# Performance work log

Measured on AMD Instinct MI355X. Metric: run time of the kernel, lower is better.

## Reference

```python
import jax, jax.numpy as jnp
import numpy as np
import math

B, L, H, NH = 4, 2048, 256, 8
DH = H // NH

def setup_inputs() -> dict:
    key = jax.random.key(0)
    ks = jax.random.split(key, 10)
    q = jax.random.normal(ks[0], (B, L, H), dtype=jnp.float32)
    k = jax.random.normal(ks[1], (B, L, H), dtype=jnp.float32)
    v = jax.random.normal(ks[2], (B, L, H), dtype=jnp.float32)
    k_b = jax.random.normal(ks[3], (B, L, H), dtype=jnp.float32)
    mask = jnp.ones((B, L), dtype=jnp.int32)
    # learned params
    scale_w = jax.random.normal(ks[4], (NH, L), dtype=jnp.float32)
    Wb = jax.random.normal(ks[5], (H, H), dtype=jnp.float32) * (1.0 / math.sqrt(H))
    bb = jnp.zeros((H,), dtype=jnp.float32)
    Ww = jax.random.normal(ks[6], (H, H), dtype=jnp.float32) * (1.0 / math.sqrt(H))
    bw = jnp.zeros((H,), dtype=jnp.float32)
    return {"q": q, "k": k, "v": v, "k_b": k_b, "mask": mask,
            "scale_w": scale_w, "Wb": Wb, "bb": bb, "Ww": Ww, "bw": bw}

def _split_heads(x):
    b, l, _ = x.shape
    return x.reshape(b, l, NH, DH).transpose(0, 2, 1, 3)  # [B, NH, L, DH]

def reference(q, k, v, k_b, mask, scale_w, Wb, bb, Ww, bw):
    qh = _split_heads(q)
    kh = _split_heads(k)
    vh = _split_heads(v)
    kb = _split_heads(k_b @ Wb.T + bb)
    # dual QK^T: [B, NH, L, L]
    corr = jnp.einsum('bhqd,bhkd->bhqk', qh, kh) + jnp.einsum('bhqd,bhkd->bhqk', qh, kb)
    corr = corr * (1.0 / math.sqrt(DH))
    # per-head, per-query-position learned scale
    corr = corr * scale_w[None, :, :, None]
    # mask over key positions: [B,1,1,L]
    corr = jnp.where(mask[:, None, None, :] == 0, jnp.float32(-1e9), corr)
    prob = jax.nn.softmax(corr, axis=-1)
    hidden = jnp.einsum('bhqk,bhkd->bhqd', prob, vh)  # [B, NH, L, DH]
    hidden = hidden.transpose(0, 2, 1, 3).reshape(hidden.shape[0], -1, NH * DH)
    return hidden @ Ww.T + bw
```

## Files before the change

kernel.cpp:

```cpp
#include <hip/hip_runtime.h>
#include <stdint.h>
#include <stddef.h>


#define B_ 4
#define L_ 2048
#define H_ 256
#define NH_ 8
#define DH_ 32

typedef float    f32x4  __attribute__((ext_vector_type(4)));
typedef float    f32x16 __attribute__((ext_vector_type(16)));
typedef __bf16   bf16x8 __attribute__((ext_vector_type(8)));
typedef uint16_t u16x4  __attribute__((ext_vector_type(4)));
typedef uint16_t u16x8  __attribute__((ext_vector_type(8)));

static __device__ __forceinline__ uint16_t f2bf(float f) {
  __bf16 h = (__bf16)f;
  return __builtin_bit_cast(uint16_t, h);
}

static __device__ __forceinline__ void gl16(const void* g, void* l) {
  __builtin_amdgcn_global_load_lds(
      (const __attribute__((address_space(1))) uint32_t*)g,
      (__attribute__((address_space(3))) uint32_t*)l, 16, 0, 0);
}

#define OFF_KSUM 0
#define OFF_VTP  (OFF_KSUM + (size_t)B_*NH_*L_*DH_*2)
#define OFF_HID  (OFF_VTP  + (size_t)B_*NH_*L_*DH_*2)


__global__ __launch_bounds__(256, 2) void wv_k(const float* __restrict__ v,
                                               uint16_t* __restrict__ vtp) {
  __shared__ uint16_t T[128][33];
  const int tid = threadIdx.x;
  const int bh = blockIdx.x >> 4, t = blockIdx.x & 15;
  const int b = bh >> 3, h = bh & 7;
  {
    int r = tid >> 1, half = tid & 1;
    const float* src = v + ((size_t)(b * 2048 + t * 128 + r)) * 256 + h * 32 + half * 16;
    f32x4 s0 = *(const f32x4*)(src);
    f32x4 s1 = *(const f32x4*)(src + 4);
    f32x4 s2 = *(const f32x4*)(src + 8);
    f32x4 s3 = *(const f32x4*)(src + 12);
#pragma unroll
    for (int i = 0; i < 4; i++) {
      T[r][half * 16 + i]      = f2bf(s0[i]);
      T[r][half * 16 + 4 + i]  = f2bf(s1[i]);
      T[r][half * 16 + 8 + i]  = f2bf(s2[i]);
      T[r][half * 16 + 12 + i] = f2bf(s3[i]);
    }
  }
  __syncthreads();
#pragma unroll
  for (int rep = 0; rep < 2; rep++) {
    int gid = rep * 256 + tid;
    int slot = gid >> 5, d = gid & 31;
    int kg = slot >> 2, s = (slot >> 1) & 1, hii = slot & 1;
    u16x8 val;
#pragma unroll
    for (int e = 0; e < 8; e++) {
      int key = kg * 32 + s * 16 + 4 * hii + (e & 3) + 8 * (e >> 2);
      val[e] = T[key][d];
    }
    *(u16x8*)(vtp + (size_t)bh * 65536 + t * 4096 + slot * 256 + d * 8) = val;
  }
}

__global__ __launch_bounds__(512, 1) void ksum_k(const float* __restrict__ kb,
                                                 const float* __restrict__ wb,
                                                 const float* __restrict__ kin,
                                                 const float* __restrict__ bb,
                                                 uint16_t* __restrict__ ksum_out) {
  __shared__ uint16_t WB[65536];
  const int tid = threadIdx.x;
  const int mblk = blockIdx.x;
  const int wv = tid >> 6, lane = tid & 63;
  const int g = lane >> 4, qi = lane & 15;
  const int rt = wv & 1, ch = wv >> 1;
  const int m = mblk * 32 + rt * 16 + qi;
  const int n0 = ch * 64;

#pragma unroll
  for (int s = 0; s < 16; s++) {
    int gid = s * 512 + tid;
    int n = gid >> 5, gl = gid & 31;
    const float* src = wb + (size_t)n * 256 + gl * 8;
    f32x4 a0 = *(const f32x4*)src;
    f32x4 a1 = *(const f32x4*)(src + 4);
    u16x8 val;
#pragma unroll
    for (int i = 0; i < 4; i++) { val[i] = f2bf(a0[i]); val[4 + i] = f2bf(a1[i]); }
    *(u16x8*)&WB[n * 256 + (gl ^ (n & 7)) * 8] = val;
  }
  __syncthreads();

  f32x4 acc[4];
#pragma unroll
  for (int i = 0; i < 4; i++) acc[i] = (f32x4){0.f, 0.f, 0.f, 0.f};

#pragma unroll
  for (int ks = 0; ks < 8; ks++) {
    const float* ap = kb + (size_t)m * 256 + ks * 32 + g * 8;
    f32x4 a0 = *(const f32x4*)ap;
    f32x4 a1 = *(const f32x4*)(ap + 4);
    bf16x8 af;
#pragma unroll
    for (int i = 0; i < 4; i++) { af[i] = (__bf16)a0[i]; af[4 + i] = (__bf16)a1[i]; }
#pragma unroll
    for (int nt = 0; nt < 4; nt++) {
      int n = n0 + nt * 16 + qi;
      bf16x8 bf = *(const bf16x8*)&WB[n * 256 + ((ks * 4 + g) ^ (n & 7)) * 8];
      acc[nt] = __builtin_amdgcn_mfma_f32_16x16x32_bf16(af, bf, acc[nt], 0, 0, 0);
    }
  }
#pragma unroll
  for (int nt = 0; nt < 4; nt++) {
    int n = n0 + nt * 16 + qi;
    float bbv = bb[n];
    int h = n >> 5, d = n & 31;
#pragma unroll
    for (int j = 0; j < 4; j++) {
      int mr = mblk * 32 + rt * 16 + g * 4 + j;
      float val = acc[nt][j] + bbv + kin[(size_t)mr * 256 + n];
      int bq = mr >> 11, l = mr & 2047;
      size_t off = (size_t)(bq * 8 + h) * 65536 +
                   (l >> 5) * 1024 + (d >> 4) * 512 + (l & 31) * 16 + (d & 15);
      ksum_out[off] = f2bf(val);
    }
  }
}

__global__ __launch_bounds__(512, 2) void attn_k(const float* __restrict__ q,
                                                 const int* __restrict__ mask,
                                                 const float* __restrict__ scale_w,
                                                 const uint16_t* __restrict__ ksum,
                                                 const uint16_t* __restrict__ vtp,
                                                 uint16_t* __restrict__ hid) {
  __shared__ __align__(16) uint16_t KV[2][8192];
  __shared__ int anyz;

  const int bid = blockIdx.x;
  const int bh = bid & 31, qblk = bid >> 5;
  const int b = bh >> 3, h = bh & 7;
  const int tid = threadIdx.x, wv = tid >> 6, lane = tid & 63;
  const int qi = lane & 31, hi = lane >> 5;
  const int qrow = qblk * 256 + wv * 32 + qi;

  const float scale = scale_w[h * 2048 + qrow] * (0.17677669529663687f * 1.4426950408889634f);
  const float* qp = q + ((size_t)(b * 2048 + qrow)) * 256 + h * 32;
  bf16x8 qf0, qf1;
  {
    f32x4 a0 = *(const f32x4*)(qp + hi * 8);
    f32x4 a1 = *(const f32x4*)(qp + hi * 8 + 4);
    f32x4 c0 = *(const f32x4*)(qp + 16 + hi * 8);
    f32x4 c1 = *(const f32x4*)(qp + 16 + hi * 8 + 4);
#pragma unroll
    for (int i = 0; i < 4; i++) {
      qf0[i] = (__bf16)(a0[i] * scale); qf0[4 + i] = (__bf16)(a1[i] * scale);
      qf1[i] = (__bf16)(c0[i] * scale); qf1[4 + i] = (__bf16)(c1[i] * scale);
    }
  }

  const uint16_t* kbase = ksum + (size_t)bh * 65536;
  const uint16_t* vbase = vtp + (size_t)bh * 65536;

  if (tid == 0) anyz = 0;
  __syncthreads();
  {
    int bad = 0;
#pragma unroll
    for (int i = 0; i < 4; i++) bad |= (mask[b * 2048 + tid * 4 + i] == 0);
    if (bad) anyz = 1;
  }
  __syncthreads();
  const bool allmask = (anyz == 0);

#define STAGE(tt, bufp)                                                            \
  {                                                                                \
    gl16(kbase + (tt) * 4096 + wv * 512 + lane * 8, (bufp) + wv * 512);            \
    gl16(vbase + (tt) * 4096 + wv * 512 + lane * 8, (bufp) + 4096 + wv * 512);     \
  }
  STAGE(0, &KV[0][0]);
  STAGE(1, &KV[1][0]);

  float lsa[4] = {0.f, 0.f, 0.f, 0.f};
  f32x16 Oa, Ob, Z0;
#pragma unroll
  for (int i = 0; i < 16; i++) { Oa[i] = 0.f; Ob[i] = 0.f; Z0[i] = 0.f; }

  for (int t = 0; t < 16; t++) {
    uint16_t* bufp = &KV[t & 1][0];
    if (t < 15) { asm volatile("s_waitcnt vmcnt(2)" ::: "memory"); }
    else        { asm volatile("s_waitcnt vmcnt(0)" ::: "memory"); }
    __builtin_amdgcn_sched_barrier(0);
    __builtin_amdgcn_s_barrier();

    const uint16_t* Kl = bufp;
    const uint16_t* Vl = bufp + 4096;
#pragma unroll
    for (int kg = 0; kg < 4; kg++) {
      bf16x8 kf0 = *(const bf16x8*)&Kl[kg * 1024 + qi * 16 + hi * 8];
      bf16x8 kf1 = *(const bf16x8*)&Kl[kg * 1024 + 512 + qi * 16 + hi * 8];
      f32x16 S;
      __builtin_amdgcn_s_setprio(1);
      S = __builtin_amdgcn_mfma_f32_32x32x16_bf16(kf0, qf0, Z0, 0, 0, 0);
      S = __builtin_amdgcn_mfma_f32_32x32x16_bf16(kf1, qf1, S, 0, 0, 0);
      __builtin_amdgcn_s_setprio(0);

      if (!allmask) {
        const int* mrow = mask + b * 2048 + t * 128 + kg * 32 + 4 * hi;
#pragma unroll
        for (int r = 0; r < 16; r++)
          if (mrow[(r & 3) + 8 * (r >> 2)] == 0) S[r] = -1.0e9f;
      }

      bf16x8 pa0, pa1;
#pragma unroll
      for (int r = 0; r < 8; r++) {
        float p = __builtin_amdgcn_exp2f(S[r]);
        pa0[r] = (__bf16)p;
        lsa[r & 3] += p;
      }
#pragma unroll
      for (int r = 0; r < 8; r++) {
        float p = __builtin_amdgcn_exp2f(S[8 + r]);
        pa1[r] = (__bf16)p;
        lsa[r & 3] += p;
      }

      bf16x8 vf0 = *(const bf16x8*)&Vl[(kg * 4 + hi) * 256 + qi * 8];
      bf16x8 vf1 = *(const bf16x8*)&Vl[(kg * 4 + 2 + hi) * 256 + qi * 8];
      __builtin_amdgcn_s_setprio(1);
      Oa = __builtin_amdgcn_mfma_f32_32x32x16_bf16(vf0, pa0, Oa, 0, 0, 0);
      Ob = __builtin_amdgcn_mfma_f32_32x32x16_bf16(vf1, pa1, Ob, 0, 0, 0);
      __builtin_amdgcn_s_setprio(0);
    }

    __builtin_amdgcn_s_barrier();
    if (t < 14) STAGE(t + 2, bufp);
  }
#undef STAGE

  float l = (lsa[0] + lsa[1]) + (lsa[2] + lsa[3]);
  l += __shfl_xor(l, 32);
  const float inv = 1.0f / l;
  uint16_t* hp = hid + ((size_t)(b * 2048 + qrow)) * 256 + h * 32;
#pragma unroll
  for (int grp = 0; grp < 4; grp++) {
    u16x4 st;
#pragma unroll
    for (int j = 0; j < 4; j++) st[j] = f2bf((Oa[grp * 4 + j] + Ob[grp * 4 + j]) * inv);
    *(u16x4*)(hp + grp * 8 + hi * 4) = st;
  }
}

__global__ __launch_bounds__(512, 1) void oproj_k(const uint16_t* __restrict__ hid,
                                                  const float* __restrict__ ww,
                                                  const float* __restrict__ bw,
                                                  float* __restrict__ out) {
  __shared__ uint16_t WW[65536];
  const int tid = threadIdx.x;
  const int mblk = blockIdx.x;
  const int wv = tid >> 6, lane = tid & 63;
  const int g = lane >> 4, qi = lane & 15;
  const int rt = wv & 1, ch = wv >> 1;
  const int m = mblk * 32 + rt * 16 + qi;
  const int n0 = ch * 64;

#pragma unroll
  for (int s = 0; s < 16; s++) {
    int gid = s * 512 + tid;
    int n = gid >> 5, gl = gid & 31;
    const float* src = ww + (size_t)n * 256 + gl * 8;
    f32x4 a0 = *(const f32x4*)src;
    f32x4 a1 = *(const f32x4*)(src + 4);
    u16x8 val;
#pragma unroll
    for (int i = 0; i < 4; i++) { val[i] = f2bf(a0[i]); val[4 + i] = f2bf(a1[i]); }
    *(u16x8*)&WW[n * 256 + (gl ^ (n & 7)) * 8] = val;
  }
  __syncthreads();

  f32x4 acc[4];
#pragma unroll
  for (int i = 0; i < 4; i++) acc[i] = (f32x4){0.f, 0.f, 0.f, 0.f};

#pragma unroll
  for (int ks = 0; ks < 8; ks++) {
    bf16x8 af = *(const bf16x8*)(hid + (size_t)m * 256 + ks * 32 + g * 8);
#pragma unroll
    for (int nt = 0; nt < 4; nt++) {
      int n = n0 + nt * 16 + qi;
      bf16x8 bf = *(const bf16x8*)&WW[n * 256 + ((ks * 4 + g) ^ (n & 7)) * 8];
      acc[nt] = __builtin_amdgcn_mfma_f32_16x16x32_bf16(af, bf, acc[nt], 0, 0, 0);
    }
  }
#pragma unroll
  for (int nt = 0; nt < 4; nt++) {
    int n = n0 + nt * 16 + qi;
    float bwv = bw[n];
#pragma unroll
    for (int j = 0; j < 4; j++) {
      int mr = mblk * 32 + rt * 16 + g * 4 + j;
      out[(size_t)mr * 256 + n] = acc[nt][j] + bwv;
    }
  }
}

extern "C" void kernel_launch(void* const* d_in, const int* in_sizes, int n_in,
                              void* d_out, int out_size, void* d_ws, size_t ws_size,
                              hipStream_t stream) {
  const float* q       = (const float*)d_in[0];
  const float* k       = (const float*)d_in[1];
  const float* v       = (const float*)d_in[2];
  const float* kb      = (const float*)d_in[3];
  const int*   mask    = (const int*)d_in[4];
  const float* scale_w = (const float*)d_in[5];
  const float* Wb      = (const float*)d_in[6];
  const float* bb      = (const float*)d_in[7];
  const float* Ww      = (const float*)d_in[8];
  const float* bw      = (const float*)d_in[9];

  char* ws = (char*)d_ws;
  uint16_t* ksum  = (uint16_t*)(ws + OFF_KSUM);
  uint16_t* vtp   = (uint16_t*)(ws + OFF_VTP);
  uint16_t* hid   = (uint16_t*)(ws + OFF_HID);
  float* out = (float*)d_out;

  wv_k<<<dim3(512), dim3(256), 0, stream>>>(v, vtp);
  ksum_k<<<dim3(256), dim3(512), 0, stream>>>(kb, Wb, k, bb, ksum);
  attn_k<<<dim3(256), dim3(512), 0, stream>>>(q, mask, scale_w, ksum, vtp, hid);
  oproj_k<<<dim3(256), dim3(512), 0, stream>>>(hid, Ww, bw, out);
}
```

Measured before the change: 52.03 us.

## Merge V-transpose and K-sum prep kernels; halve attention block size

Folds the V transpose/convert kernel into the K-sum projection kernel as extra blocks of a single launch, removing one kernel launch and letting both workloads run concurrently. The attention kernel now uses 256-thread blocks covering 128 query rows each, doubling the grid to 512 blocks for better CU coverage, with each wave issuing twice as many async K/V stage loads and waiting on a larger vmcnt. The V blocks now carry the large 128KB LDS allocation sized for the GEMM path, which may limit their occupancy. Halving the block size also doubles total K/V tile traffic per head.

```diff
diff --git a/kernel.cpp b/kernel.cpp
--- a/kernel.cpp
+++ b/kernel.cpp
@@ -31,51 +31,48 @@
 #define OFF_HID  (OFF_VTP  + (size_t)B_*NH_*L_*DH_*2)
 
 
-__global__ __launch_bounds__(256, 2) void wv_k(const float* __restrict__ v,
-                                               uint16_t* __restrict__ vtp) {
-  __shared__ uint16_t T[128][33];
-  const int tid = threadIdx.x;
-  const int bh = blockIdx.x >> 4, t = blockIdx.x & 15;
-  const int b = bh >> 3, h = bh & 7;
-  {
-    int r = tid >> 1, half = tid & 1;
-    const float* src = v + ((size_t)(b * 2048 + t * 128 + r)) * 256 + h * 32 + half * 16;
-    f32x4 s0 = *(const f32x4*)(src);
-    f32x4 s1 = *(const f32x4*)(src + 4);
-    f32x4 s2 = *(const f32x4*)(src + 8);
-    f32x4 s3 = *(const f32x4*)(src + 12);
-#pragma unroll
-    for (int i = 0; i < 4; i++) {
-      T[r][half * 16 + i]      = f2bf(s0[i]);
-      T[r][half * 16 + 4 + i]  = f2bf(s1[i]);
-      T[r][half * 16 + 8 + i]  = f2bf(s2[i]);
-      T[r][half * 16 + 12 + i] = f2bf(s3[i]);
-    }
-  }
-  __syncthreads();
-#pragma unroll
-  for (int rep = 0; rep < 2; rep++) {
-    int gid = rep * 256 + tid;
-    int slot = gid >> 5, d = gid & 31;
-    int kg = slot >> 2, s = (slot >> 1) & 1, hii = slot & 1;
-    u16x8 val;
-#pragma unroll
-    for (int e = 0; e < 8; e++) {
-      int key = kg * 32 + s * 16 + 4 * hii + (e & 3) + 8 * (e >> 2);
-      val[e] = T[key][d];
-    }
-    *(u16x8*)(vtp + (size_t)bh * 65536 + t * 4096 + slot * 256 + d * 8) = val;
-  }
-}
-
-__global__ __launch_bounds__(512, 1) void ksum_k(const float* __restrict__ kb,
+__global__ __launch_bounds__(512, 1) void prep_k(const float* __restrict__ kb,
                                                  const float* __restrict__ wb,
                                                  const float* __restrict__ kin,
                                                  const float* __restrict__ bb,
-                                                 uint16_t* __restrict__ ksum_out) {
-  __shared__ uint16_t WB[65536];
+                                                 const float* __restrict__ v,
+                                                 uint16_t* __restrict__ ksum_out,
+                                                 uint16_t* __restrict__ vtp) {
+  __shared__ uint16_t SM[65536];
   const int tid = threadIdx.x;
-  const int mblk = blockIdx.x;
+
+  if (blockIdx.x < 512) {
+    uint16_t (*T)[33] = (uint16_t(*)[33])SM;
+    const int bh = blockIdx.x >> 4, t = blockIdx.x & 15;
+    const int b = bh >> 3, h = bh & 7;
+    {
+      int r = tid >> 2, qtr = tid & 3;
+      const float* src = v + ((size_t)(b * 2048 + t * 128 + r)) * 256 + h * 32 + qtr * 8;
+      f32x4 s0 = *(const f32x4*)(src);
+      f32x4 s1 = *(const f32x4*)(src + 4);
+#pragma unroll
+      for (int i = 0; i < 4; i++) {
+        T[r][qtr * 8 + i]     = f2bf(s0[i]);
+        T[r][qtr * 8 + 4 + i] = f2bf(s1[i]);
+      }
+    }
+    __syncthreads();
+    {
+      int slot = tid >> 5, d = tid & 31;
+      int kg = slot >> 2, s = (slot >> 1) & 1, hii = slot & 1;
+      u16x8 val;
+#pragma unroll
+      for (int e = 0; e < 8; e++) {
+        int key = kg * 32 + s * 16 + 4 * hii + (e & 3) + 8 * (e >> 2);
+        val[e] = T[key][d];
+      }
+      *(u16x8*)(vtp + (size_t)bh * 65536 + t * 4096 + slot * 256 + d * 8) = val;
+    }
+    return;
+  }
+
+  uint16_t* WB = SM;
+  const int mblk = blockIdx.x - 512;
   const int wv = tid >> 6, lane = tid & 63;
   const int g = lane >> 4, qi = lane & 15;
   const int rt = wv & 1, ch = wv >> 1;
@@ -132,7 +129,7 @@
   }
 }
 
-__global__ __launch_bounds__(512, 2) void attn_k(const float* __restrict__ q,
+__global__ __launch_bounds__(256, 2) void attn_k(const float* __restrict__ q,
                                                  const int* __restrict__ mask,
                                                  const float* __restrict__ scale_w,
                                                  const uint16_t* __restrict__ ksum,
@@ -146,7 +143,7 @@
   const int b = bh >> 3, h = bh & 7;
   const int tid = threadIdx.x, wv = tid >> 6, lane = tid & 63;
   const int qi = lane & 31, hi = lane >> 5;
-  const int qrow = qblk * 256 + wv * 32 + qi;
+  const int qrow = qblk * 128 + wv * 32 + qi;
 
   const float scale = scale_w[h * 2048 + qrow] * (0.17677669529663687f * 1.4426950408889634f);
   const float* qp = q + ((size_t)(b * 2048 + qrow)) * 256 + h * 32;
@@ -171,16 +168,19 @@
   {
     int bad = 0;
 #pragma unroll
-    for (int i = 0; i < 4; i++) bad |= (mask[b * 2048 + tid * 4 + i] == 0);
+    for (int i = 0; i < 8; i++) bad |= (mask[b * 2048 + tid * 8 + i] == 0);
     if (bad) anyz = 1;
   }
   __syncthreads();
   const bool allmask = (anyz == 0);
 
-#define STAGE(tt, bufp)                                                            \
-  {                                                                                \
-    gl16(kbase + (tt) * 4096 + wv * 512 + lane * 8, (bufp) + wv * 512);            \
-    gl16(vbase + (tt) * 4096 + wv * 512 + lane * 8, (bufp) + 4096 + wv * 512);     \
+#define STAGE(tt, bufp)                                                                      \
+  {                                                                                          \
+    _Pragma("unroll")                                                                        \
+    for (int i_ = 0; i_ < 2; i_++) {                                                         \
+      gl16(kbase + (tt) * 4096 + (wv * 2 + i_) * 512 + lane * 8, (bufp) + (wv * 2 + i_) * 512); \
+      gl16(vbase + (tt) * 4096 + (wv * 2 + i_) * 512 + lane * 8, (bufp) + 4096 + (wv * 2 + i_) * 512); \
+    }                                                                                        \
   }
   STAGE(0, &KV[0][0]);
   STAGE(1, &KV[1][0]);
@@ -192,7 +192,7 @@
 
   for (int t = 0; t < 16; t++) {
     uint16_t* bufp = &KV[t & 1][0];
-    if (t < 15) { asm volatile("s_waitcnt vmcnt(2)" ::: "memory"); }
+    if (t < 15) { asm volatile("s_waitcnt vmcnt(4)" ::: "memory"); }
     else        { asm volatile("s_waitcnt vmcnt(0)" ::: "memory"); }
     __builtin_amdgcn_sched_barrier(0);
     __builtin_amdgcn_s_barrier();
@@ -329,8 +329,7 @@
   uint16_t* hid   = (uint16_t*)(ws + OFF_HID);
   float* out = (float*)d_out;
 
-  wv_k<<<dim3(512), dim3(256), 0, stream>>>(v, vtp);
-  ksum_k<<<dim3(256), dim3(512), 0, stream>>>(kb, Wb, k, bb, ksum);
-  attn_k<<<dim3(256), dim3(512), 0, stream>>>(q, mask, scale_w, ksum, vtp, hid);
+  prep_k<<<dim3(768), dim3(512), 0, stream>>>(kb, Wb, k, bb, v, ksum, vtp);
+  attn_k<<<dim3(512), dim3(256), 0, stream>>>(q, mask, scale_w, ksum, vtp, hid);
   oproj_k<<<dim3(256), dim3(512), 0, stream>>>(hid, Ww, bw, out);
 }
```

New measurement: 49.90 us. 1.04x faster.
